# Kernel optimization log

Hardware: AMD Instinct MI355X
Metric: run time of the kernel (lower is better)

## Reference

```python
import jax, jax.numpy as jnp
import numpy as np

B, D, H, L, E, NL, P, IMG, NT = 32, 768, 8, 6, 8, 256, 16, 224, 10
G = IMG // P          # 14 patches per side
NP = G * G            # 196 patches
HD = D // H           # 96 head dim
TOPK = 2
KEEP = 0.25
EPS = 1e-5


def layer_norm(x, g, b):
    m = x.mean(-1, keepdims=True)
    v = ((x - m) ** 2).mean(-1, keepdims=True)
    return (x - m) / jnp.sqrt(v + EPS) * g + b


def mha(q, kv, in_w, in_b, out_w, out_b):
    # torch nn.MultiheadAttention: packed in_proj (3D, D), out_proj (D, D)
    wq, wk, wv = in_w[:D], in_w[D:2 * D], in_w[2 * D:]
    bq, bk, bv = in_b[:D], in_b[D:2 * D], in_b[2 * D:]

    def heads(x, w, b):
        y = x @ w.T + b                               # (B, S, D)
        return y.reshape(x.shape[0], x.shape[1], H, HD).transpose(0, 2, 1, 3)

    Q = heads(q, wq, bq)
    K = heads(kv, wk, bk)
    V = heads(kv, wv, bv)
    scores = jnp.einsum('bhqd,bhkd->bhqk', Q, K) / np.sqrt(HD).astype(np.float32)
    attn = jax.nn.softmax(scores, axis=-1)
    o = jnp.einsum('bhqk,bhkd->bhqd', attn, V)
    o = o.transpose(0, 2, 1, 3).reshape(q.shape[0], q.shape[1], D)
    return o @ out_w.T + out_b


def moe(x, rw, rb, w1, b1, w2, b2):
    # top-2 routing; renormalize the top-k weights with a second softmax
    Bq, S, _ = x.shape
    T = Bq * S
    xt = x.reshape(T, D)
    probs = jax.nn.softmax(xt @ rw.T + rb, axis=-1)       # (T, E)
    tw, ti = jax.lax.top_k(probs, TOPK)                   # (T, K)
    tw = jax.nn.softmax(tw, axis=-1)
    # combine weights per expert: (T, E), >0 only for the chosen experts
    combine = (jax.nn.one_hot(ti, E, dtype=x.dtype) * tw[..., None]).sum(axis=1)
    out = jnp.zeros_like(xt)
    for e in range(E):  # fixed small expert count
        h = jax.nn.gelu(xt @ w1[e].T + b1[e], approximate=False)
        out = out + (h @ w2[e].T + b2[e]) * combine[:, e:e + 1]
    return out.reshape(Bq, S, D)


def _forward(images, type_ids, mask_noise, conv_w, conv_b, pos_emb, type_emb,
             latents, ca_in_w, ca_in_b, ca_out_w, ca_out_b, ca_ln_g, ca_ln_b,
             sa_in_w, sa_in_b, sa_out_w, sa_out_b, ln1_g, ln1_b,
             router_w, router_b, e_w1, e_b1, e_w2, e_b2, ln2_g, ln2_b):
    b = images.shape[0]
    # non-overlapping conv patch embed == unfold + matmul
    xp = images.reshape(b, 3, G, P, G, P).transpose(0, 2, 4, 1, 3, 5)
    xp = xp.reshape(b, NP, 3 * P * P)
    patches = xp @ conv_w.reshape(D, -1).T + conv_b        # (B, NP, D)
    patches = patches + pos_emb + type_emb[type_ids][:, None, :]
    # random masking: keep n_visible patches chosen by argsort of noise
    n_visible = int(NP * KEEP)
    order = jnp.argsort(mask_noise, axis=1)
    visible_indices = order[:, :n_visible]
    masked_indices = order[:, n_visible:]
    visible = jnp.take_along_axis(patches, visible_indices[:, :, None], axis=1)
    # cross attention from latents to visible patches
    lat = jnp.broadcast_to(latents, (b, NL, D))
    lat = layer_norm(lat + mha(lat, visible, ca_in_w, ca_in_b, ca_out_w, ca_out_b),
                     ca_ln_g, ca_ln_b)
    for l in range(L):
        a = mha(lat, lat, sa_in_w[l], sa_in_b[l], sa_out_w[l], sa_out_b[l])
        lat = layer_norm(lat + a, ln1_g[l], ln1_b[l])
        m = moe(lat, router_w[l], router_b[l], e_w1[l], e_b1[l], e_w2[l], e_b2[l])
        lat = layer_norm(lat + m, ln2_g[l], ln2_b[l])
    return lat, visible_indices, masked_indices


def setup_inputs() -> dict:
    key = jax.random.key(0)
    ks = jax.random.split(key, 16)
    r = lambda k, shape, s=0.02: jax.random.normal(k, shape, dtype=jnp.float32) * s
    z = lambda shape: jnp.zeros(shape, jnp.float32)
    o = lambda shape: jnp.ones(shape, jnp.float32)
    inp = {}
    inp['images'] = jax.random.normal(ks[0], (B, 3, IMG, IMG), dtype=jnp.float32)
    inp['type_ids'] = jax.random.randint(ks[1], (B,), 0, NT)
    inp['mask_noise'] = jax.random.uniform(ks[2], (B, NP), dtype=jnp.float32)
    inp['conv_w'] = r(ks[3], (D, 3, P, P))
    inp['conv_b'] = z((D,))
    inp['pos_emb'] = r(ks[4], (1, NP, D), 1.0)
    inp['type_emb'] = r(ks[5], (NT, D), 1.0)
    inp['latents'] = r(ks[6], (NL, D), 1.0)
    inp['ca_in_w'] = r(ks[7], (3 * D, D)); inp['ca_in_b'] = z((3 * D,))
    inp['ca_out_w'] = r(ks[8], (D, D)); inp['ca_out_b'] = z((D,))
    inp['ca_ln_g'] = o((D,)); inp['ca_ln_b'] = z((D,))
    inp['sa_in_w'] = r(ks[9], (L, 3 * D, D)); inp['sa_in_b'] = z((L, 3 * D))
    inp['sa_out_w'] = r(ks[10], (L, D, D)); inp['sa_out_b'] = z((L, D))
    inp['ln1_g'] = o((L, D)); inp['ln1_b'] = z((L, D))
    inp['router_w'] = r(ks[11], (L, E, D)); inp['router_b'] = z((L, E))
    inp['e_w1'] = r(ks[12], (L, E, 2 * D, D)); inp['e_b1'] = z((L, E, 2 * D))
    inp['e_w2'] = r(ks[13], (L, E, D, 2 * D)); inp['e_b2'] = z((L, E, D))
    inp['ln2_g'] = o((L, D)); inp['ln2_b'] = z((L, D))
    return inp


def reference(images, type_ids, mask_noise, conv_w, conv_b, pos_emb, type_emb,
              latents, ca_in_w, ca_in_b, ca_out_w, ca_out_b, ca_ln_g, ca_ln_b,
              sa_in_w, sa_in_b, sa_out_w, sa_out_b, ln1_g, ln1_b,
              router_w, router_b, e_w1, e_b1, e_w2, e_b2, ln2_g, ln2_b):
    return _forward(images, type_ids, mask_noise, conv_w, conv_b, pos_emb,
                    type_emb, latents, ca_in_w, ca_in_b, ca_out_w, ca_out_b,
                    ca_ln_g, ca_ln_b, sa_in_w, sa_in_b, sa_out_w, sa_out_b,
                    ln1_g, ln1_b, router_w, router_b, e_w1, e_b1, e_w2, e_b2,
                    ln2_g, ln2_b)
```

## Files before the change

kernel.cpp:

```cpp
#include <hip/hip_runtime.h>

typedef unsigned short u16;
typedef unsigned int u32;
typedef __attribute__((ext_vector_type(8))) u16 u16x8;
typedef __attribute__((ext_vector_type(8))) __bf16 bf16x8;
typedef __attribute__((ext_vector_type(4))) float f32x4;

#define DEV static __device__ __forceinline__

DEV float b2f(u16 u){ unsigned int i = ((unsigned int)u)<<16; float f; __builtin_memcpy(&f,&i,4); return f; }
DEV u16 f2b(float f){ unsigned int x; __builtin_memcpy(&x,&f,4); x = x + 0x7fffu + ((x>>16)&1u); return (u16)(x>>16); }

DEV void gll16(const u16* g, u16* l){
    __builtin_amdgcn_global_load_lds(
        (const __attribute__((address_space(1))) u32*)(const void*)g,
        (__attribute__((address_space(3))) u32*)(void*)l, 16, 0, 0);
}

template<bool F32>
DEV u16x8 ld8(const void* base, long off){
    if constexpr (F32){
        const float* p = (const float*)base + off;
        float4 a = *(const float4*)p;
        float4 b = *(const float4*)(p+4);
        u16x8 r;
        r[0]=f2b(a.x); r[1]=f2b(a.y); r[2]=f2b(a.z); r[3]=f2b(a.w);
        r[4]=f2b(b.x); r[5]=f2b(b.y); r[6]=f2b(b.z); r[7]=f2b(b.w);
        return r;
    } else {
        return *(const u16x8*)((const u16*)base + off);
    }
}
template<bool F32>
DEV const void* vadd(const void* p, long elems){
    if constexpr (F32) return (const void*)((const float*)p + elems);
    else               return (const void*)((const u16*)p + elems);
}

#define LAT_ELEMS 6291456
#define NVIS 49
#define NMASK 147
#define T_TOK 8192
#define MOE_CAP 17408
#define MOE_HALF 8704
#define KOFF 6291456L
#define VOFF 12582912L

__global__ __launch_bounds__(256) void wconv(const float* __restrict__ src, u16* __restrict__ dst, long n)
{
    long i = ((long)blockIdx.x*256 + threadIdx.x)*8;
    if (i >= n) return;
    *(u16x8*)(dst + i) = ld8<true>(src, i);
}

__global__ __launch_bounds__(256) void argsort_k(const float* __restrict__ noise,
                                                 int* __restrict__ order,
                                                 float* __restrict__ dout)
{
    __shared__ float vals[196];
    __shared__ int ord[196];
    int b = blockIdx.x, tid = threadIdx.x;
    if (tid < 196) vals[tid] = noise[b*196 + tid];
    __syncthreads();
    if (tid < 196){
        float vi = vals[tid]; int rank = 0;
        for (int j=0;j<196;j++){ float vj = vals[j]; rank += (vj < vi) || (vj == vi && j < tid); }
        ord[rank] = tid;
    }
    __syncthreads();
    if (tid < 196){
        int v = ord[tid];
        order[b*196 + tid] = v;
        if (tid < NVIS) dout[LAT_ELEMS + b*NVIS + tid] = (float)v;
        else            dout[LAT_ELEMS + 32*NVIS + b*NMASK + (tid - NVIS)] = (float)v;
    }
}

__global__ __launch_bounds__(256) void patch_gather(const float* __restrict__ images,
                                                    const int* __restrict__ order,
                                                    u16* __restrict__ Ap)
{
    int i = blockIdx.x*256 + threadIdx.x;
    int t = i/48, kc = i - t*48;
    if (t >= 1664) return;
    if (t >= 1568){
        u16x8 z{};
        *(u16x8*)(Ap + (long)t*768 + kc*16)     = z;
        *(u16x8*)(Ap + (long)t*768 + kc*16 + 8) = z;
        return;
    }
    int b = t/49, vi = t - b*49;
    int p = order[b*196 + vi];
    int c = kc >> 4, py = kc & 15;
    int gy = p/14, gx = p - gy*14;
    const float* src = images + (((long)(b*3 + c)*224 + gy*16 + py)*224 + gx*16);
    u16x8 o0 = ld8<true>(src, 0);
    u16x8 o1 = ld8<true>(src, 8);
    *(u16x8*)(Ap + (long)t*768 + kc*16)     = o0;
    *(u16x8*)(Ap + (long)t*768 + kc*16 + 8) = o1;
}

__global__ __launch_bounds__(256) void add_pos_type(u16* __restrict__ vis,
                                                    const int* __restrict__ order,
                                                    const int* __restrict__ type_ids,
                                                    const float* __restrict__ pos,
                                                    const float* __restrict__ temb)
{
    int i = blockIdx.x*256 + threadIdx.x;
    int t = i/96, dc = (i - t*96)*8;
    if (t >= 1568) return;
    int b = t/49, vi = t - b*49;
    int p = order[b*196 + vi], tb = type_ids[b];
    u16x8 a = *(u16x8*)(vis + (long)t*768 + dc);
    const float* pp = pos  + (long)p*768 + dc;
    const float* tt = temb + (long)tb*768 + dc;
    float4 p0 = *(const float4*)pp, p1 = *(const float4*)(pp+4);
    float4 t0 = *(const float4*)tt, t1 = *(const float4*)(tt+4);
    u16x8 o;
    o[0]=f2b(b2f(a[0])+p0.x+t0.x); o[1]=f2b(b2f(a[1])+p0.y+t0.y);
    o[2]=f2b(b2f(a[2])+p0.z+t0.z); o[3]=f2b(b2f(a[3])+p0.w+t0.w);
    o[4]=f2b(b2f(a[4])+p1.x+t1.x); o[5]=f2b(b2f(a[5])+p1.y+t1.y);
    o[6]=f2b(b2f(a[6])+p1.z+t1.z); o[7]=f2b(b2f(a[7])+p1.w+t1.w);
    *(u16x8*)(vis + (long)t*768 + dc) = o;
}

template<int BK, bool BIAS, bool GELU, int GRP, bool AF32, bool BF32, bool SWZ, bool GLL>
__global__ __launch_bounds__(256,4) void gemm_nt(
    const void* __restrict__ A, const void* __restrict__ B, const float* __restrict__ bias,
    u16* __restrict__ C,
    int M, int N, int K, int lda, int ldb, int ldc,
    float scale, int ZLO, int NB,
    long sAh, long sAl, long sBh, long sBl, long sCh, long sCl,
    const int* __restrict__ aoff, const int* __restrict__ tos, const u16* __restrict__ zbuf,
    int row_base, long sBE, long sBiasE)
{
    int bx = blockIdx.x, by = blockIdx.y;
    if (SWZ){
        int nx = gridDim.x, ny = gridDim.y;
        int nwg = nx*ny;
        int flat = by*nx + bx;
        int q = nwg >> 3, r = nwg & 7;
        int xcd = flat & 7, idx = flat >> 3;
        int wg = (xcd < r ? xcd*(q+1) : r*(q+1) + (xcd - r)*q) + idx;
        bx = wg % nx; by = wg / nx;
    }
    int z = blockIdx.z; int zh = z / ZLO, zl = z - zh*ZLO;
    const void* Ab = vadd<AF32>(A, zh*sAh + zl*sAl);
    const void* Bb = vadd<BF32>(B, zh*sBh + zl*sBl);
    u16* Cb = C + zh*sCh + zl*sCl;
    const float* biasb = bias;
    int row0 = by*128, col0 = bx*128;
    int lim = 0;
    if (GRP == 1 || GRP == 2){
        lim = aoff[8];
        int g0 = row_base + row0;
        if (g0 >= lim) return;
        int e = 0;
        #pragma unroll
        for (int i=1;i<8;i++) if (g0 >= aoff[i]) e = i;
        Bb = vadd<BF32>(B, (long)e*sBE);
        if (BIAS) biasb = bias + (long)e*sBiasE;
    }
    constexpr int SP = GLL ? BK : BK + 8;
    __shared__ __align__(16) u16 As[128*SP];
    __shared__ __align__(16) u16 Bs[128*SP];
    int tid = threadIdx.x;
    int lane = tid & 63, wv = tid >> 6;
    int wr = (wv>>1)*64, wc = (wv&1)*64;
    f32x4 acc[4][4];
    #pragma unroll
    for (int m=0;m<4;m++){
        #pragma unroll
        for (int n=0;n<4;n++) acc[m][n] = f32x4{0.f,0.f,0.f,0.f};
    }
    constexpr int RPC = BK/8;
    constexpr int RPI = 64/RPC;
    constexpr int NJ  = 32/RPI;
    constexpr int PER = 128*RPC/256;
    int tA[4];
    if (GRP == 1){
        if (GLL){
            #pragma unroll
            for (int j=0;j<NJ;j++){
                int r = wv*32 + j*RPI + (lane/RPC);
                tA[j] = tos[row_base + row0 + r];
            }
        } else {
            #pragma unroll
            for (int j=0;j<PER && j<4;j++){
                int c = j*256 + tid;
                tA[j] = tos[row_base + row0 + c/RPC];
            }
        }
    }
    for (int k0=0; k0<K; k0+=BK){
        if constexpr (GLL){
            #pragma unroll
            for (int j=0;j<NJ;j++){
                int r  = wv*32 + j*RPI + (lane/RPC);
                int ch = lane % RPC;
                const u16* sa;
                if (GRP == 1){
                    int t = tA[j];
                    sa = (t >= 0) ? (const u16*)Ab + (long)t*lda + k0 + ch*8 : zbuf + ch*8;
                } else {
                    sa = (const u16*)Ab + (long)(row0+r)*lda + k0 + ch*8;
                }
                gll16(sa, As + (wv*32 + j*RPI)*BK);
                const u16* sb = (col0 + r < NB) ? (const u16*)Bb + (long)(col0+r)*ldb + k0 + ch*8
                                                : zbuf + ch*8;
                gll16(sb, Bs + (wv*32 + j*RPI)*BK);
            }
        } else {
            #pragma unroll
            for (int j=0;j<PER;j++){
                int c = j*256 + tid;
                int r = c / RPC, cc = (c - r*RPC)*8;
                u16x8 va{}, vb{};
                if (GRP == 1){
                    int t = tA[j];
                    if (t >= 0) va = ld8<AF32>(Ab, (long)t*lda + k0 + cc);
                } else {
                    va = ld8<AF32>(Ab, (long)(row0+r)*lda + k0 + cc);
                }
                if (col0 + r < NB) vb = ld8<BF32>(Bb, (long)(col0+r)*ldb + k0 + cc);
                *(u16x8*)(As + r*SP + cc) = va;
                *(u16x8*)(Bs + r*SP + cc) = vb;
            }
        }
        __syncthreads();
        #pragma unroll
        for (int kk=0; kk<BK/32; kk++){
            bf16x8 af[4], bg[4];
            #pragma unroll
            for (int m=0;m<4;m++)
                af[m] = *(const bf16x8*)(As + (wr + m*16 + (lane&15))*SP + kk*32 + (lane>>4)*8);
            #pragma unroll
            for (int n=0;n<4;n++)
                bg[n] = *(const bf16x8*)(Bs + (wc + n*16 + (lane&15))*SP + kk*32 + (lane>>4)*8);
            #pragma unroll
            for (int m=0;m<4;m++){
                #pragma unroll
                for (int n=0;n<4;n++)
                    acc[m][n] = __builtin_amdgcn_mfma_f32_16x16x32_bf16(af[m], bg[n], acc[m][n], 0,0,0);
            }
        }
        __syncthreads();
    }
    #pragma unroll
    for (int m=0;m<4;m++){
        int rbase = row0 + wr + m*16 + ((lane>>4)<<2);
        #pragma unroll
        for (int n=0;n<4;n++){
            int col = col0 + wc + n*16 + (lane&15);
            if (col < N){
                float bv = BIAS ? biasb[col] : 0.f;
                #pragma unroll
                for (int j=0;j<4;j++){
                    int row = rbase + j;
                    bool ok = (row < M);
                    if (GRP == 1 || GRP == 2) ok = ok && (row_base + row) < lim;
                    if (ok){
                        float v = acc[m][n][j]*scale + bv;
                        if (GELU) v = 0.5f*v*(1.f + erff(v*0.70710678118f));
                        u16 ov = f2b(v);
                        if (GRP == 3){
                            if (col < 768){
                                Cb[(long)row*768 + col] = ov;
                            } else if (col < 1536){
                                Cb[sBE + (long)row*768 + (col - 768)] = ov;
                            } else {
                                int c96 = col - 1536;
                                int h = c96/96, d = c96 - h*96;
                                Cb[sBiasE + ((long)((row>>8)*8 + h)*96 + d)*256 + (row & 255)] = ov;
                            }
                        } else if (GRP == 2){
                            Cb[(long)(row_base + row)*ldc + col] = ov;
                        } else {
                            Cb[(long)row*ldc + col] = ov;
                        }
                    }
                }
            }
        }
    }
}

__global__ __launch_bounds__(256) void ca_attn(const u16* __restrict__ Qc,
                                               const u16* __restrict__ KV,
                                               u16* __restrict__ attn_out)
{
    __shared__ float Sm[256*49];
    __shared__ u16 KVs[49*96];
    int b = blockIdx.x, h = blockIdx.y, q = threadIdx.x;
    for (int i=q; i<49*96; i+=256){ int k=i/96, d=i-k*96; KVs[i] = KV[(long)(b*49+k)*1536 + h*96 + d]; }
    __syncthreads();
    float qv[96];
    #pragma unroll
    for (int d=0;d<96;d++) qv[d] = b2f(Qc[(long)q*768 + h*96 + d]);
    for (int k=0;k<49;k++){
        float a = 0.f;
        #pragma unroll
        for (int d=0;d<96;d++) a += qv[d]*b2f(KVs[k*96+d]);
        Sm[q*49+k] = a*0.10206207f;
    }
    __syncthreads();
    for (int i=q; i<49*96; i+=256){ int k=i/96, d=i-k*96; KVs[i] = KV[(long)(b*49+k)*1536 + 768 + h*96 + d]; }
    float mx = -1e30f;
    for (int k=0;k<49;k++) mx = fmaxf(mx, Sm[q*49+k]);
    float sum = 0.f;
    for (int k=0;k<49;k++){ float e = __expf(Sm[q*49+k]-mx); Sm[q*49+k]=e; sum+=e; }
    float inv = 1.f/sum;
    __syncthreads();
    for (int d=0;d<96;d++){
        float a = 0.f;
        for (int k=0;k<49;k++) a += Sm[q*49+k]*b2f(KVs[k*96+d]);
        attn_out[(long)(b*256+q)*768 + h*96 + d] = f2b(a*inv);
    }
}

__global__ __launch_bounds__(256) void softmax256(u16* __restrict__ S, int rows)
{
    int wid = threadIdx.x >> 6, lane = threadIdx.x & 63;
    int r = blockIdx.x*4 + wid; if (r >= rows) return;
    u16* p = S + (long)r*256;
    ushort4 v = *(const ushort4*)(p + lane*4);
    float x0=b2f(v.x), x1=b2f(v.y), x2=b2f(v.z), x3=b2f(v.w);
    float mx = fmaxf(fmaxf(x0,x1), fmaxf(x2,x3));
    #pragma unroll
    for (int off=32; off>=1; off>>=1) mx = fmaxf(mx, __shfl_xor(mx, off, 64));
    x0=__expf(x0-mx); x1=__expf(x1-mx); x2=__expf(x2-mx); x3=__expf(x3-mx);
    float s = x0+x1+x2+x3;
    #pragma unroll
    for (int off=32; off>=1; off>>=1) s += __shfl_xor(s, off, 64);
    float inv = 1.f/s;
    ushort4 o; o.x=f2b(x0*inv); o.y=f2b(x1*inv); o.z=f2b(x2*inv); o.w=f2b(x3*inv);
    *(ushort4*)(p + lane*4) = o;
}

template<int MODE>
__global__ __launch_bounds__(256) void ln_k(
    const float* __restrict__ res, int resmod,
    const u16* __restrict__ add,
    const u16* __restrict__ OutE, const int* __restrict__ sot, const float2* __restrict__ w01,
    const float* __restrict__ g, const float* __restrict__ bb,
    float* __restrict__ out, u16* __restrict__ outb, int T)
{
    int wid = threadIdx.x >> 6, lane = threadIdx.x & 63;
    int t = blockIdx.x*4 + wid; if (t >= T) return;
    const float* rp = res + (long)(t % resmod)*768;
    float x[12];
    #pragma unroll
    for (int j=0;j<3;j++){
        float4 v = *(const float4*)(rp + j*256 + lane*4);
        x[j*4+0]=v.x; x[j*4+1]=v.y; x[j*4+2]=v.z; x[j*4+3]=v.w;
    }
    if (MODE == 0){
        const u16* ap = add + (long)t*768;
        #pragma unroll
        for (int j=0;j<3;j++){
            ushort4 v = *(const ushort4*)(ap + j*256 + lane*4);
            x[j*4+0]+=b2f(v.x); x[j*4+1]+=b2f(v.y); x[j*4+2]+=b2f(v.z); x[j*4+3]+=b2f(v.w);
        }
    } else {
        int s0 = sot[2*t], s1 = sot[2*t+1];
        float2 w = w01[t];
        const u16* p0 = OutE + (long)s0*768;
        const u16* p1 = OutE + (long)s1*768;
        #pragma unroll
        for (int j=0;j<3;j++){
            ushort4 v0 = *(const ushort4*)(p0 + j*256 + lane*4);
            ushort4 v1 = *(const ushort4*)(p1 + j*256 + lane*4);
            x[j*4+0] += w.x*b2f(v0.x) + w.y*b2f(v1.x);
            x[j*4+1] += w.x*b2f(v0.y) + w.y*b2f(v1.y);
            x[j*4+2] += w.x*b2f(v0.z) + w.y*b2f(v1.z);
            x[j*4+3] += w.x*b2f(v0.w) + w.y*b2f(v1.w);
        }
    }
    float s = 0.f;
    #pragma unroll
    for (int i=0;i<12;i++) s += x[i];
    #pragma unroll
    for (int off=32; off>=1; off>>=1) s += __shfl_xor(s, off, 64);
    float m = s*(1.f/768.f);
    float s2 = 0.f;
    #pragma unroll
    for (int i=0;i<12;i++){ float d = x[i]-m; s2 += d*d; }
    #pragma unroll
    for (int off=32; off>=1; off>>=1) s2 += __shfl_xor(s2, off, 64);
    float rstd = rsqrtf(s2*(1.f/768.f) + 1e-5f);
    #pragma unroll
    for (int j=0;j<3;j++){
        int col = j*256 + lane*4;
        float4 gg = *(const float4*)(g + col);
        float4 bv = *(const float4*)(bb + col);
        float4 o;
        o.x = (x[j*4+0]-m)*rstd*gg.x + bv.x;
        o.y = (x[j*4+1]-m)*rstd*gg.y + bv.y;
        o.z = (x[j*4+2]-m)*rstd*gg.z + bv.z;
        o.w = (x[j*4+3]-m)*rstd*gg.w + bv.w;
        *(float4*)(out + (long)t*768 + col) = o;
        if (outb != nullptr){
            ushort4 ob;
            ob.x = f2b(o.x); ob.y = f2b(o.y); ob.z = f2b(o.z); ob.w = f2b(o.w);
            *(ushort4*)(outb + (long)t*768 + col) = ob;
        }
    }
}

__global__ __launch_bounds__(256) void router_k(const float* __restrict__ lat,
                                                const float* __restrict__ rw, const float* __restrict__ rb,
                                                int2* __restrict__ e01, float2* __restrict__ w01)
{
    int wid = threadIdx.x >> 6, lane = threadIdx.x & 63;
    int t = blockIdx.x*4 + wid; if (t >= T_TOK) return;
    const float* lp = lat + (long)t*768;
    float4 x[3];
    #pragma unroll
    for (int j=0;j<3;j++) x[j] = *(const float4*)(lp + j*256 + lane*4);
    float part[8];
    #pragma unroll
    for (int e=0;e<8;e++){
        const float* wp = rw + e*768;
        float a = 0.f;
        #pragma unroll
        for (int j=0;j<3;j++){
            float4 w4 = *(const float4*)(wp + j*256 + lane*4);
            a += x[j].x*w4.x + x[j].y*w4.y + x[j].z*w4.z + x[j].w*w4.w;
        }
        part[e] = a;
    }
    #pragma unroll
    for (int e=0;e<8;e++){
        #pragma unroll
        for (int off=32; off>=1; off>>=1) part[e] += __shfl_xor(part[e], off, 64);
    }
    if (lane == 0){
        float pe[8];
        float mx = -1e30f;
        #pragma unroll
        for (int e=0;e<8;e++){ pe[e] = part[e] + rb[e]; mx = fmaxf(mx, pe[e]); }
        float sum = 0.f;
        #pragma unroll
        for (int e=0;e<8;e++){ pe[e] = __expf(pe[e]-mx); sum += pe[e]; }
        float inv = 1.f/sum;
        #pragma unroll
        for (int e=0;e<8;e++) pe[e] *= inv;
        int i0 = 0;
        #pragma unroll
        for (int e=1;e<8;e++) if (pe[e] > pe[i0]) i0 = e;
        int i1 = -1;
        for (int e=0;e<8;e++){ if (e == i0) continue; if (i1 < 0 || pe[e] > pe[i1]) i1 = e; }
        float ex = __expf(pe[i1] - pe[i0]);
        float w0 = 1.f/(1.f+ex), w1 = ex/(1.f+ex);
        e01[t] = int2{i0, i1};
        w01[t] = float2{w0, w1};
    }
}

__global__ __launch_bounds__(256) void route_build(const int2* __restrict__ e01,
                                                   int* __restrict__ aoff_g,
                                                   int* __restrict__ tos, int* __restrict__ sot,
                                                   u16* __restrict__ zbuf)
{
    __shared__ int wsum[8][4];
    __shared__ int wbase[8][4];
    __shared__ int aoff_s[9];
    int tid = threadIdx.x, lane = tid & 63, wid = tid >> 6;
    for (int s = tid; s < MOE_CAP; s += 256) tos[s] = -1;
    if (tid < 128) zbuf[tid] = 0;
    int t0 = tid * 32;
    int lc[8];
    #pragma unroll
    for (int e=0;e<8;e++) lc[e] = 0;
    for (int i=0;i<32;i++){
        int2 e = e01[t0+i];
        lc[e.x]++; lc[e.y]++;
    }
    int excl[8];
    #pragma unroll
    for (int e=0;e<8;e++){
        int sc = lc[e];
        #pragma unroll
        for (int off=1; off<64; off<<=1){
            int n = __shfl_up(sc, off, 64);
            if (lane >= off) sc += n;
        }
        excl[e] = sc - lc[e];
        if (lane == 63) wsum[e][wid] = sc;
    }
    __syncthreads();
    if (tid == 0){
        int tot = 0;
        #pragma unroll
        for (int e=0;e<8;e++){
            int s = 0;
            #pragma unroll
            for (int w=0;w<4;w++){ wbase[e][w] = s; s += wsum[e][w]; }
            aoff_s[e] = tot;
            tot += (s + 127) & ~127;
        }
        aoff_s[8] = tot;
        #pragma unroll
        for (int e=0;e<9;e++) aoff_g[e] = aoff_s[e];
    }
    __syncthreads();
    int cur[8];
    #pragma unroll
    for (int e=0;e<8;e++) cur[e] = aoff_s[e] + wbase[e][wid] + excl[e];
    for (int i=0;i<32;i++){
        int t = t0 + i;
        int2 e = e01[t];
        int s0 = cur[e.x]++;
        tos[s0] = t; sot[2*t]   = s0;
        int s1 = cur[e.y]++;
        tos[s1] = t; sot[2*t+1] = s1;
    }
}

extern "C" void kernel_launch(void* const* d_in, const int* in_sizes, int n_in,
                              void* d_out, int out_size, void* d_ws, size_t ws_size,
                              hipStream_t stream)
{
    (void)in_sizes; (void)n_in; (void)out_size;
    const float* images   = (const float*)d_in[0];
    const int*   type_ids = (const int*)d_in[1];
    const float* noise    = (const float*)d_in[2];
    const float* conv_w   = (const float*)d_in[3];
    const float* conv_b   = (const float*)d_in[4];
    const float* pos_emb  = (const float*)d_in[5];
    const float* type_emb = (const float*)d_in[6];
    const float* latents  = (const float*)d_in[7];
    const float* ca_in_w  = (const float*)d_in[8];
    const float* ca_in_b  = (const float*)d_in[9];
    const float* ca_out_w = (const float*)d_in[10];
    const float* ca_out_b = (const float*)d_in[11];
    const float* ca_ln_g  = (const float*)d_in[12];
    const float* ca_ln_b  = (const float*)d_in[13];
    const float* sa_in_w  = (const float*)d_in[14];
    const float* sa_in_b  = (const float*)d_in[15];
    const float* sa_out_w = (const float*)d_in[16];
    const float* sa_out_b = (const float*)d_in[17];
    const float* ln1_g    = (const float*)d_in[18];
    const float* ln1_b    = (const float*)d_in[19];
    const float* router_w = (const float*)d_in[20];
    const float* router_b = (const float*)d_in[21];
    const float* e_w1     = (const float*)d_in[22];
    const float* e_b1     = (const float*)d_in[23];
    const float* e_w2     = (const float*)d_in[24];
    const float* e_b2     = (const float*)d_in[25];
    const float* ln2_g    = (const float*)d_in[26];
    const float* ln2_b    = (const float*)d_in[27];
    float* dout = (float*)d_out;
    float* lat  = dout;

    char* p = (char*)d_ws;
    auto alloc = [&](size_t n)->char*{ char* r = p; p += (n + 255) & ~(size_t)255; return r; };
    int*    order  = (int*)   alloc(32*196*4);
    int2*   e01    = (int2*)  alloc((size_t)T_TOK*8);
    float2* w01    = (float2*)alloc((size_t)T_TOK*8);
    int*    aoff   = (int*)   alloc(64);
    int*    tos    = (int*)   alloc((size_t)MOE_CAP*4);
    int*    sot    = (int*)   alloc((size_t)T_TOK*2*4);
    u16*    zbuf   = (u16*)   alloc(256);
    size_t aux_used = (size_t)(p - (char*)d_ws);
    const size_t WB_BYTES = 92798976ull + 260702208ull;
    bool wb  = ws_size >= aux_used + WB_BYTES;
    bool big = wb || ws_size >= aux_used + 92798976ull;
    u16* ar = (u16*)alloc(wb ? WB_BYTES : (big ? 92798976ull : 71303168ull));
    u16* latb   = big ? ar : nullptr;
    u16* common = big ? ar + 6291456 : ar;
    u16* wbufA  = wb ? ar + 6291456 + 40108032 : nullptr;
    u16* Ap  = common;
    u16* vis = common + 1277952;
    u16* KV  = common + 2555904;
    u16* Qc  = common + 5111808;
    u16* caO = common + 5308416;
    u16* caM = common + 11599872;
    u16* Qb  = common;
    u16* Vt  = common + VOFF;
    u16* S   = common + 18874368;
    u16* aO  = common;
    u16* mha = common + KOFF;
    u16* Hbuf = common;
    u16* OutE = common + (big ? 26738688 : 13369344);
    u16* cwb      = wbufA;
    u16* cainb    = wbufA + 589824;
    u16* caoutb   = wbufA + 2359296;
    u16* winbAll  = wbufA + 2949120;
    u16* woutbAll = wbufA + 13565952;
    u16* w1bAll   = wbufA + 17104896;
    u16* w2bAll   = wbufA + 73728000;

    const float ONE = 1.0f;
    const float SCL = 0.10206207f;
    const long Z0 = 0;

    argsort_k<<<32, 256, 0, stream>>>(noise, order, dout);
    patch_gather<<<312, 256, 0, stream>>>(images, order, Ap);
    if (wb){
        wconv<<<288, 256, 0, stream>>>(conv_w, cwb, 589824);
        wconv<<<864, 256, 0, stream>>>(ca_in_w, cainb, 1769472);
        wconv<<<288, 256, 0, stream>>>(ca_out_w, caoutb, 589824);
        wconv<<<5184, 256, 0, stream>>>(sa_in_w, winbAll, 10616832);
        wconv<<<1728, 256, 0, stream>>>(sa_out_w, woutbAll, 3538944);
        wconv<<<27648, 256, 0, stream>>>(e_w1, w1bAll, 56623104);
        wconv<<<27648, 256, 0, stream>>>(e_w2, w2bAll, 56623104);
        gemm_nt<64,true,false,0,false,false,true,true><<<dim3(6,13,1),256,0,stream>>>(Ap, cwb, conv_b, vis,
            1664,768,768, 768,768,768, ONE, 1, 768, Z0,Z0,Z0,Z0,Z0,Z0, nullptr,nullptr,zbuf,0, Z0,Z0);
        add_pos_type<<<588, 256, 0, stream>>>(vis, order, type_ids, pos_emb, type_emb);
        gemm_nt<64,true,false,0,true,false,true,false><<<dim3(6,2,1),256,0,stream>>>(latents, cainb, ca_in_b, Qc,
            256,768,768, 768,768,768, ONE, 1, 768, Z0,Z0,Z0,Z0,Z0,Z0, nullptr,nullptr,zbuf,0, Z0,Z0);
        gemm_nt<64,true,false,0,false,false,true,true><<<dim3(12,13,1),256,0,stream>>>(vis, cainb + 589824, ca_in_b + 768, KV,
            1664,1536,768, 768,768,1536, ONE, 1, 1536, Z0,Z0,Z0,Z0,Z0,Z0, nullptr,nullptr,zbuf,0, Z0,Z0);
        ca_attn<<<dim3(32,8), 256, 0, stream>>>(Qc, KV, caO);
        gemm_nt<64,true,false,0,false,false,true,true><<<dim3(6,64,1),256,0,stream>>>(caO, caoutb, ca_out_b, caM,
            T_TOK,768,768, 768,768,768, ONE, 1, 768, Z0,Z0,Z0,Z0,Z0,Z0, nullptr,nullptr,zbuf,0, Z0,Z0);
    } else {
        gemm_nt<64,true,false,0,false,true,false,false><<<dim3(6,13,1),256,0,stream>>>(Ap, conv_w, conv_b, vis,
            1664,768,768, 768,768,768, ONE, 1, 768, Z0,Z0,Z0,Z0,Z0,Z0, nullptr,nullptr,zbuf,0, Z0,Z0);
        add_pos_type<<<588, 256, 0, stream>>>(vis, order, type_ids, pos_emb, type_emb);
        gemm_nt<64,true,false,0,true,true,false,false><<<dim3(6,2,1),256,0,stream>>>(latents, ca_in_w, ca_in_b, Qc,
            256,768,768, 768,768,768, ONE, 1, 768, Z0,Z0,Z0,Z0,Z0,Z0, nullptr,nullptr,zbuf,0, Z0,Z0);
        gemm_nt<64,true,false,0,false,true,false,false><<<dim3(12,13,1),256,0,stream>>>(vis, ca_in_w + 768*768, ca_in_b + 768, KV,
            1664,1536,768, 768,768,1536, ONE, 1, 1536, Z0,Z0,Z0,Z0,Z0,Z0, nullptr,nullptr,zbuf,0, Z0,Z0);
        ca_attn<<<dim3(32,8), 256, 0, stream>>>(Qc, KV, caO);
        gemm_nt<64,true,false,0,false,true,false,false><<<dim3(6,64,1),256,0,stream>>>(caO, ca_out_w, ca_out_b, caM,
            T_TOK,768,768, 768,768,768, ONE, 1, 768, Z0,Z0,Z0,Z0,Z0,Z0, nullptr,nullptr,zbuf,0, Z0,Z0);
    }
    ln_k<0><<<2048, 256, 0, stream>>>(latents, 256, caM, nullptr,nullptr,nullptr, ca_ln_g, ca_ln_b, lat, latb, T_TOK);

    for (int l=0; l<6; l++){
        const float* b_in  = sa_in_b  + l*2304;
        const float* b_out = sa_out_b + l*768;
        const float* b1 = e_b1 + l*8*1536;
        const float* b2 = e_b2 + l*8*768;
        if (wb){
            const u16* winb  = winbAll  + (long)l*1769472;
            const u16* woutb = woutbAll + (long)l*589824;
            const u16* w1b   = w1bAll   + (long)l*9437184;
            const u16* w2b   = w2bAll   + (long)l*9437184;
            gemm_nt<64,true,false,3,false,false,true,true><<<dim3(18,64,1),256,0,stream>>>(latb, winb, b_in, Qb,
                T_TOK,2304,768, 768,768,0, ONE, 1, 2304, Z0,Z0,Z0,Z0,Z0,Z0, nullptr,nullptr,zbuf,0, KOFF, VOFF);
            gemm_nt<32,false,false,0,false,false,false,true><<<dim3(2,2,256),256,0,stream>>>(Qb, Qb + KOFF, nullptr, S,
                256,256,96, 768,768,256, SCL, 8, 256, 196608,96, 196608,96, 524288,65536, nullptr,nullptr,zbuf,0, Z0,Z0);
            softmax256<<<16384, 256, 0, stream>>>(S, 65536);
            gemm_nt<64,false,false,0,false,false,false,true><<<dim3(1,2,256),256,0,stream>>>(S, Vt, nullptr, aO,
                256,96,256, 256,256,768, ONE, 8, 96, 524288,65536, 196608,24576, 196608,96, nullptr,nullptr,zbuf,0, Z0,Z0);
            gemm_nt<64,true,false,0,false,false,true,true><<<dim3(6,64,1),256,0,stream>>>(aO, woutb, b_out, mha,
                T_TOK,768,768, 768,768,768, ONE, 1, 768, Z0,Z0,Z0,Z0,Z0,Z0, nullptr,nullptr,zbuf,0, Z0,Z0);
            ln_k<0><<<2048, 256, 0, stream>>>(lat, T_TOK, mha, nullptr,nullptr,nullptr, ln1_g + l*768, ln1_b + l*768, lat, latb, T_TOK);
            router_k<<<2048, 256, 0, stream>>>(lat, router_w + l*8*768, router_b + l*8, e01, w01);
            route_build<<<1, 256, 0, stream>>>(e01, aoff, tos, sot, zbuf);
            gemm_nt<64,true,true,1,false,false,true,true><<<dim3(12,136,1),256,0,stream>>>(latb, w1b, b1, Hbuf,
                MOE_CAP,1536,768, 768,768,1536, ONE, 1, 1536, Z0,Z0,Z0,Z0,Z0,Z0,
                aoff, tos, zbuf, 0, (long)1536*768, 1536);
            gemm_nt<64,true,false,2,false,false,true,true><<<dim3(6,136,1),256,0,stream>>>(Hbuf, w2b, b2, OutE,
                MOE_CAP,768,1536, 1536,1536,768, ONE, 1, 768, Z0,Z0,Z0,Z0,Z0,Z0,
                aoff, tos, zbuf, 0, (long)768*1536, 768);
            ln_k<1><<<2048, 256, 0, stream>>>(lat, T_TOK, nullptr, OutE, sot, w01, ln2_g + l*768, ln2_b + l*768, lat, latb, T_TOK);
        } else {
            const float* w_in  = sa_in_w  + (long)l*2304*768;
            const float* w_out = sa_out_w + (long)l*768*768;
            const float* w1 = e_w1 + (long)l*8*1536*768;
            const float* w2 = e_w2 + (long)l*8*768*1536;
            if (big){
                gemm_nt<64,true,false,3,false,true,false,false><<<dim3(18,64,1),256,0,stream>>>(latb, w_in, b_in, Qb,
                    T_TOK,2304,768, 768,768,0, ONE, 1, 2304, Z0,Z0,Z0,Z0,Z0,Z0, nullptr,nullptr,zbuf,0, KOFF, VOFF);
            } else {
                gemm_nt<64,true,false,3,true,true,false,false><<<dim3(18,64,1),256,0,stream>>>(lat, w_in, b_in, Qb,
                    T_TOK,2304,768, 768,768,0, ONE, 1, 2304, Z0,Z0,Z0,Z0,Z0,Z0, nullptr,nullptr,zbuf,0, KOFF, VOFF);
            }
            gemm_nt<32,false,false,0,false,false,false,false><<<dim3(2,2,256),256,0,stream>>>(Qb, Qb + KOFF, nullptr, S,
                256,256,96, 768,768,256, SCL, 8, 256, 196608,96, 196608,96, 524288,65536, nullptr,nullptr,zbuf,0, Z0,Z0);
            softmax256<<<16384, 256, 0, stream>>>(S, 65536);
            gemm_nt<64,false,false,0,false,false,false,false><<<dim3(1,2,256),256,0,stream>>>(S, Vt, nullptr, aO,
                256,96,256, 256,256,768, ONE, 8, 96, 524288,65536, 196608,24576, 196608,96, nullptr,nullptr,zbuf,0, Z0,Z0);
            gemm_nt<64,true,false,0,false,true,false,false><<<dim3(6,64,1),256,0,stream>>>(aO, w_out, b_out, mha,
                T_TOK,768,768, 768,768,768, ONE, 1, 768, Z0,Z0,Z0,Z0,Z0,Z0, nullptr,nullptr,zbuf,0, Z0,Z0);
            ln_k<0><<<2048, 256, 0, stream>>>(lat, T_TOK, mha, nullptr,nullptr,nullptr, ln1_g + l*768, ln1_b + l*768, lat, latb, T_TOK);
            router_k<<<2048, 256, 0, stream>>>(lat, router_w + l*8*768, router_b + l*8, e01, w01);
            route_build<<<1, 256, 0, stream>>>(e01, aoff, tos, sot, zbuf);
            if (big){
                gemm_nt<64,true,true,1,false,true,false,false><<<dim3(12,136,1),256,0,stream>>>(latb, w1, b1, Hbuf,
                    MOE_CAP,1536,768, 768,768,1536, ONE, 1, 1536, Z0,Z0,Z0,Z0,Z0,Z0,
                    aoff, tos, zbuf, 0, (long)1536*768, 1536);
                gemm_nt<64,true,false,2,false,true,false,false><<<dim3(6,136,1),256,0,stream>>>(Hbuf, w2, b2, OutE,
                    MOE_CAP,768,1536, 1536,1536,768, ONE, 1, 768, Z0,Z0,Z0,Z0,Z0,Z0,
                    aoff, tos, zbuf, 0, (long)768*1536, 768);
            } else {
                for (int rb2=0; rb2<MOE_CAP; rb2+=MOE_HALF){
                    gemm_nt<64,true,true,1,true,true,false,false><<<dim3(12,68,1),256,0,stream>>>(lat, w1, b1, Hbuf,
                        MOE_HALF,1536,768, 768,768,1536, ONE, 1, 1536, Z0,Z0,Z0,Z0,Z0,Z0,
                        aoff, tos, zbuf, rb2, (long)1536*768, 1536);
                    gemm_nt<64,true,false,2,false,true,false,false><<<dim3(6,68,1),256,0,stream>>>(Hbuf, w2, b2, OutE,
                        MOE_HALF,768,1536, 1536,1536,768, ONE, 1, 768, Z0,Z0,Z0,Z0,Z0,Z0,
                        aoff, tos, zbuf, rb2, (long)768*1536, 768);
                }
            }
            ln_k<1><<<2048, 256, 0, stream>>>(lat, T_TOK, nullptr, OutE, sot, w01, ln2_g + l*768, ln2_b + l*768, lat, latb, T_TOK);
        }
    }
}
```

Baseline: 2.528 ms.

## Fuse attention scores with softmax and layernorm with router

Adds a dedicated MFMA kernel that computes the self-attention QK^T scores for a 128x256 tile per head and applies the row softmax in registers before writing. This replaces the separate scores GEMM and softmax256 launch and removes one round trip of the score matrix through memory. The router projection and top-2 selection move into the post-attention layernorm kernel, reusing the normalized values already in registers instead of rereading lat. It also raises the gemm occupancy hint to 5 and zeroes zbuf in argsort. The occupancy hint may force register spilling, and the fused kernel keeps a 128-entry accumulator per thread.

```diff
diff --git a/kernel.cpp b/kernel.cpp
--- a/kernel.cpp
+++ b/kernel.cpp
@@ -55,11 +55,13 @@
 
 __global__ __launch_bounds__(256) void argsort_k(const float* __restrict__ noise,
                                                  int* __restrict__ order,
-                                                 float* __restrict__ dout)
+                                                 float* __restrict__ dout,
+                                                 u16* __restrict__ zbuf)
 {
     __shared__ float vals[196];
     __shared__ int ord[196];
     int b = blockIdx.x, tid = threadIdx.x;
+    if (b == 0 && tid < 128) zbuf[tid] = 0;
     if (tid < 196) vals[tid] = noise[b*196 + tid];
     __syncthreads();
     if (tid < 196){
@@ -125,7 +127,7 @@
 }
 
 template<int BK, bool BIAS, bool GELU, int GRP, bool AF32, bool BF32, bool SWZ, bool GLL>
-__global__ __launch_bounds__(256,4) void gemm_nt(
+__global__ __launch_bounds__(256,5) void gemm_nt(
     const void* __restrict__ A, const void* __restrict__ B, const float* __restrict__ bias,
     u16* __restrict__ C,
     int M, int N, int K, int lda, int ldb, int ldc,
@@ -286,6 +288,72 @@
     }
 }
 
+__global__ __launch_bounds__(256,2) void scores_sm(const u16* __restrict__ Q,
+                                                   const u16* __restrict__ K,
+                                                   u16* __restrict__ S)
+{
+    __shared__ __align__(16) u16 As[128*32];
+    __shared__ __align__(16) u16 Bs[256*32];
+    int z = blockIdx.y;
+    int b = z >> 3, h = z & 7;
+    const u16* Ab = Q + (long)b*196608 + h*96 + (long)blockIdx.x*128*768;
+    const u16* Bb = K + (long)b*196608 + h*96;
+    int tid = threadIdx.x, lane = tid & 63, wv = tid >> 6;
+    f32x4 acc[2][16];
+    #pragma unroll
+    for (int m=0;m<2;m++){
+        #pragma unroll
+        for (int n=0;n<16;n++) acc[m][n] = f32x4{0.f,0.f,0.f,0.f};
+    }
+    int ch = lane & 3, rr = lane >> 2;
+    for (int k0=0;k0<96;k0+=32){
+        #pragma unroll
+        for (int j=0;j<2;j++){
+            int r = wv*32 + j*16 + rr;
+            gll16(Ab + (long)r*768 + k0 + ch*8, As + (wv*128 + j*64)*8);
+        }
+        #pragma unroll
+        for (int j=0;j<4;j++){
+            int r = wv*64 + j*16 + rr;
+            gll16(Bb + (long)r*768 + k0 + ch*8, Bs + (wv*256 + j*64)*8);
+        }
+        __syncthreads();
+        bf16x8 af[2];
+        #pragma unroll
+        for (int m=0;m<2;m++)
+            af[m] = *(const bf16x8*)(As + (wv*32 + m*16 + (lane&15))*32 + (lane>>4)*8);
+        #pragma unroll
+        for (int n=0;n<16;n++){
+            bf16x8 bg = *(const bf16x8*)(Bs + (n*16 + (lane&15))*32 + (lane>>4)*8);
+            acc[0][n] = __builtin_amdgcn_mfma_f32_16x16x32_bf16(af[0], bg, acc[0][n], 0,0,0);
+            acc[1][n] = __builtin_amdgcn_mfma_f32_16x16x32_bf16(af[1], bg, acc[1][n], 0,0,0);
+        }
+        __syncthreads();
+    }
+    const float SCL = 0.10206207f;
+    u16* Sz = S + (long)z*65536 + (long)blockIdx.x*128*256;
+    #pragma unroll
+    for (int m=0;m<2;m++){
+        #pragma unroll
+        for (int j=0;j<4;j++){
+            float mx = -1e30f;
+            #pragma unroll
+            for (int n=0;n<16;n++) mx = fmaxf(mx, acc[m][n][j]);
+            #pragma unroll
+            for (int off=8; off>=1; off>>=1) mx = fmaxf(mx, __shfl_xor(mx, off, 64));
+            float ev[16]; float sum = 0.f;
+            #pragma unroll
+            for (int n=0;n<16;n++){ ev[n] = __expf((acc[m][n][j]-mx)*SCL); sum += ev[n]; }
+            #pragma unroll
+            for (int off=8; off>=1; off>>=1) sum += __shfl_xor(sum, off, 64);
+            float inv = 1.f/sum;
+            int row = wv*32 + m*16 + ((lane>>4)<<2) + j;
+            #pragma unroll
+            for (int n=0;n<16;n++) Sz[(long)row*256 + n*16 + (lane&15)] = f2b(ev[n]*inv);
+        }
+    }
+}
+
 __global__ __launch_bounds__(256) void ca_attn(const u16* __restrict__ Qc,
                                                const u16* __restrict__ KV,
                                                u16* __restrict__ attn_out)
@@ -319,31 +387,14 @@
     }
 }
 
-__global__ __launch_bounds__(256) void softmax256(u16* __restrict__ S, int rows)
-{
-    int wid = threadIdx.x >> 6, lane = threadIdx.x & 63;
-    int r = blockIdx.x*4 + wid; if (r >= rows) return;
-    u16* p = S + (long)r*256;
-    ushort4 v = *(const ushort4*)(p + lane*4);
-    float x0=b2f(v.x), x1=b2f(v.y), x2=b2f(v.z), x3=b2f(v.w);
-    float mx = fmaxf(fmaxf(x0,x1), fmaxf(x2,x3));
-    #pragma unroll
-    for (int off=32; off>=1; off>>=1) mx = fmaxf(mx, __shfl_xor(mx, off, 64));
-    x0=__expf(x0-mx); x1=__expf(x1-mx); x2=__expf(x2-mx); x3=__expf(x3-mx);
-    float s = x0+x1+x2+x3;
-    #pragma unroll
-    for (int off=32; off>=1; off>>=1) s += __shfl_xor(s, off, 64);
-    float inv = 1.f/s;
-    ushort4 o; o.x=f2b(x0*inv); o.y=f2b(x1*inv); o.z=f2b(x2*inv); o.w=f2b(x3*inv);
-    *(ushort4*)(p + lane*4) = o;
-}
-
-template<int MODE>
+template<int MODE, bool ROUTE>
 __global__ __launch_bounds__(256) void ln_k(
     const float* __restrict__ res, int resmod,
     const u16* __restrict__ add,
     const u16* __restrict__ OutE, const int* __restrict__ sot, const float2* __restrict__ w01,
     const float* __restrict__ g, const float* __restrict__ bb,
+    const float* __restrict__ rw, const float* __restrict__ rb,
+    int2* __restrict__ e01o, float2* __restrict__ w01o,
     float* __restrict__ out, u16* __restrict__ outb, int T)
 {
     int wid = threadIdx.x >> 6, lane = threadIdx.x & 63;
@@ -389,16 +440,17 @@
     #pragma unroll
     for (int off=32; off>=1; off>>=1) s2 += __shfl_xor(s2, off, 64);
     float rstd = rsqrtf(s2*(1.f/768.f) + 1e-5f);
+    float y[12];
     #pragma unroll
     for (int j=0;j<3;j++){
         int col = j*256 + lane*4;
         float4 gg = *(const float4*)(g + col);
         float4 bv = *(const float4*)(bb + col);
-        float4 o;
-        o.x = (x[j*4+0]-m)*rstd*gg.x + bv.x;
-        o.y = (x[j*4+1]-m)*rstd*gg.y + bv.y;
-        o.z = (x[j*4+2]-m)*rstd*gg.z + bv.z;
-        o.w = (x[j*4+3]-m)*rstd*gg.w + bv.w;
+        y[j*4+0] = (x[j*4+0]-m)*rstd*gg.x + bv.x;
+        y[j*4+1] = (x[j*4+1]-m)*rstd*gg.y + bv.y;
+        y[j*4+2] = (x[j*4+2]-m)*rstd*gg.z + bv.z;
+        y[j*4+3] = (x[j*4+3]-m)*rstd*gg.w + bv.w;
+        float4 o; o.x=y[j*4+0]; o.y=y[j*4+1]; o.z=y[j*4+2]; o.w=y[j*4+3];
         *(float4*)(out + (long)t*768 + col) = o;
         if (outb != nullptr){
             ushort4 ob;
@@ -406,55 +458,45 @@
             *(ushort4*)(outb + (long)t*768 + col) = ob;
         }
     }
-}
-
-__global__ __launch_bounds__(256) void router_k(const float* __restrict__ lat,
-                                                const float* __restrict__ rw, const float* __restrict__ rb,
-                                                int2* __restrict__ e01, float2* __restrict__ w01)
-{
-    int wid = threadIdx.x >> 6, lane = threadIdx.x & 63;
-    int t = blockIdx.x*4 + wid; if (t >= T_TOK) return;
-    const float* lp = lat + (long)t*768;
-    float4 x[3];
-    #pragma unroll
-    for (int j=0;j<3;j++) x[j] = *(const float4*)(lp + j*256 + lane*4);
-    float part[8];
-    #pragma unroll
-    for (int e=0;e<8;e++){
-        const float* wp = rw + e*768;
-        float a = 0.f;
-        #pragma unroll
-        for (int j=0;j<3;j++){
-            float4 w4 = *(const float4*)(wp + j*256 + lane*4);
-            a += x[j].x*w4.x + x[j].y*w4.y + x[j].z*w4.z + x[j].w*w4.w;
-        }
-        part[e] = a;
-    }
-    #pragma unroll
-    for (int e=0;e<8;e++){
-        #pragma unroll
-        for (int off=32; off>=1; off>>=1) part[e] += __shfl_xor(part[e], off, 64);
-    }
-    if (lane == 0){
-        float pe[8];
-        float mx = -1e30f;
-        #pragma unroll
-        for (int e=0;e<8;e++){ pe[e] = part[e] + rb[e]; mx = fmaxf(mx, pe[e]); }
-        float sum = 0.f;
-        #pragma unroll
-        for (int e=0;e<8;e++){ pe[e] = __expf(pe[e]-mx); sum += pe[e]; }
-        float inv = 1.f/sum;
-        #pragma unroll
-        for (int e=0;e<8;e++) pe[e] *= inv;
-        int i0 = 0;
-        #pragma unroll
-        for (int e=1;e<8;e++) if (pe[e] > pe[i0]) i0 = e;
-        int i1 = -1;
-        for (int e=0;e<8;e++){ if (e == i0) continue; if (i1 < 0 || pe[e] > pe[i1]) i1 = e; }
-        float ex = __expf(pe[i1] - pe[i0]);
-        float w0 = 1.f/(1.f+ex), w1 = ex/(1.f+ex);
-        e01[t] = int2{i0, i1};
-        w01[t] = float2{w0, w1};
+    if (ROUTE){
+        float part[8];
+        #pragma unroll
+        for (int e=0;e<8;e++){
+            const float* wp = rw + e*768;
+            float a = 0.f;
+            #pragma unroll
+            for (int j=0;j<3;j++){
+                float4 w4 = *(const float4*)(wp + j*256 + lane*4);
+                a += y[j*4+0]*w4.x + y[j*4+1]*w4.y + y[j*4+2]*w4.z + y[j*4+3]*w4.w;
+            }
+            part[e] = a;
+        }
+        #pragma unroll
+        for (int e=0;e<8;e++){
+            #pragma unroll
+            for (int off=32; off>=1; off>>=1) part[e] += __shfl_xor(part[e], off, 64);
+        }
+        if (lane == 0){
+            float pe[8];
+            float mx = -1e30f;
+            #pragma unroll
+            for (int e=0;e<8;e++){ pe[e] = part[e] + rb[e]; mx = fmaxf(mx, pe[e]); }
+            float sum = 0.f;
+            #pragma unroll
+            for (int e=0;e<8;e++){ pe[e] = __expf(pe[e]-mx); sum += pe[e]; }
+            float inv = 1.f/sum;
+            #pragma unroll
+            for (int e=0;e<8;e++) pe[e] *= inv;
+            int i0 = 0;
+            #pragma unroll
+            for (int e=1;e<8;e++) if (pe[e] > pe[i0]) i0 = e;
+            int i1 = -1;
+            for (int e=0;e<8;e++){ if (e == i0) continue; if (i1 < 0 || pe[e] > pe[i1]) i1 = e; }
+            float ex = __expf(pe[i1] - pe[i0]);
+            float w0 = 1.f/(1.f+ex), w1 = ex/(1.f+ex);
+            e01o[t] = int2{i0, i1};
+            w01o[t] = float2{w0, w1};
+        }
     }
 }
 
@@ -593,10 +635,9 @@
     u16* w2bAll   = wbufA + 73728000;
 
     const float ONE = 1.0f;
-    const float SCL = 0.10206207f;
     const long Z0 = 0;
 
-    argsort_k<<<32, 256, 0, stream>>>(noise, order, dout);
+    argsort_k<<<32, 256, 0, stream>>>(noise, order, dout, zbuf);
     patch_gather<<<312, 256, 0, stream>>>(images, order, Ap);
     if (wb){
         wconv<<<288, 256, 0, stream>>>(conv_w, cwb, 589824);
@@ -628,13 +669,16 @@
         gemm_nt<64,true,false,0,false,true,false,false><<<dim3(6,64,1),256,0,stream>>>(caO, ca_out_w, ca_out_b, caM,
             T_TOK,768,768, 768,768,768, ONE, 1, 768, Z0,Z0,Z0,Z0,Z0,Z0, nullptr,nullptr,zbuf,0, Z0,Z0);
     }
-    ln_k<0><<<2048, 256, 0, stream>>>(latents, 256, caM, nullptr,nullptr,nullptr, ca_ln_g, ca_ln_b, lat, latb, T_TOK);
+    ln_k<0,false><<<2048, 256, 0, stream>>>(latents, 256, caM, nullptr,nullptr,nullptr, ca_ln_g, ca_ln_b,
+        nullptr,nullptr,nullptr,nullptr, lat, latb, T_TOK);
 
     for (int l=0; l<6; l++){
         const float* b_in  = sa_in_b  + l*2304;
         const float* b_out = sa_out_b + l*768;
         const float* b1 = e_b1 + l*8*1536;
         const float* b2 = e_b2 + l*8*768;
+        const float* rwl = router_w + l*8*768;
+        const float* rbl = router_b + l*8;
         if (wb){
             const u16* winb  = winbAll  + (long)l*1769472;
             const u16* woutb = woutbAll + (long)l*589824;
@@ -642,15 +686,13 @@
             const u16* w2b   = w2bAll   + (long)l*9437184;
             gemm_nt<64,true,false,3,false,false,true,true><<<dim3(18,64,1),256,0,stream>>>(latb, winb, b_in, Qb,
                 T_TOK,2304,768, 768,768,0, ONE, 1, 2304, Z0,Z0,Z0,Z0,Z0,Z0, nullptr,nullptr,zbuf,0, KOFF, VOFF);
-            gemm_nt<32,false,false,0,false,false,false,true><<<dim3(2,2,256),256,0,stream>>>(Qb, Qb + KOFF, nullptr, S,
-                256,256,96, 768,768,256, SCL, 8, 256, 196608,96, 196608,96, 524288,65536, nullptr,nullptr,zbuf,0, Z0,Z0);
-            softmax256<<<16384, 256, 0, stream>>>(S, 65536);
+            scores_sm<<<dim3(2,256), 256, 0, stream>>>(Qb, Qb + KOFF, S);
             gemm_nt<64,false,false,0,false,false,false,true><<<dim3(1,2,256),256,0,stream>>>(S, Vt, nullptr, aO,
                 256,96,256, 256,256,768, ONE, 8, 96, 524288,65536, 196608,24576, 196608,96, nullptr,nullptr,zbuf,0, Z0,Z0);
             gemm_nt<64,true,false,0,false,false,true,true><<<dim3(6,64,1),256,0,stream>>>(aO, woutb, b_out, mha,
                 T_TOK,768,768, 768,768,768, ONE, 1, 768, Z0,Z0,Z0,Z0,Z0,Z0, nullptr,nullptr,zbuf,0, Z0,Z0);
-            ln_k<0><<<2048, 256, 0, stream>>>(lat, T_TOK, mha, nullptr,nullptr,nullptr, ln1_g + l*768, ln1_b + l*768, lat, latb, T_TOK);
-            router_k<<<2048, 256, 0, stream>>>(lat, router_w + l*8*768, router_b + l*8, e01, w01);
+            ln_k<0,true><<<2048, 256, 0, stream>>>(lat, T_TOK, mha, nullptr,nullptr,nullptr, ln1_g + l*768, ln1_b + l*768,
+                rwl, rbl, e01, w01, lat, latb, T_TOK);
             route_build<<<1, 256, 0, stream>>>(e01, aoff, tos, sot, zbuf);
             gemm_nt<64,true,true,1,false,false,true,true><<<dim3(12,136,1),256,0,stream>>>(latb, w1b, b1, Hbuf,
                 MOE_CAP,1536,768, 768,768,1536, ONE, 1, 1536, Z0,Z0,Z0,Z0,Z0,Z0,
@@ -658,7 +700,8 @@
             gemm_nt<64,true,false,2,false,false,true,true><<<dim3(6,136,1),256,0,stream>>>(Hbuf, w2b, b2, OutE,
                 MOE_CAP,768,1536, 1536,1536,768, ONE, 1, 768, Z0,Z0,Z0,Z0,Z0,Z0,
                 aoff, tos, zbuf, 0, (long)768*1536, 768);
-            ln_k<1><<<2048, 256, 0, stream>>>(lat, T_TOK, nullptr, OutE, sot, w01, ln2_g + l*768, ln2_b + l*768, lat, latb, T_TOK);
+            ln_k<1,false><<<2048, 256, 0, stream>>>(lat, T_TOK, nullptr, OutE, sot, w01, ln2_g + l*768, ln2_b + l*768,
+                nullptr,nullptr,nullptr,nullptr, lat, latb, T_TOK);
         } else {
             const float* w_in  = sa_in_w  + (long)l*2304*768;
             const float* w_out = sa_out_w + (long)l*768*768;
@@ -671,15 +714,13 @@
                 gemm_nt<64,true,false,3,true,true,false,false><<<dim3(18,64,1),256,0,stream>>>(lat, w_in, b_in, Qb,
                     T_TOK,2304,768, 768,768,0, ONE, 1, 2304, Z0,Z0,Z0,Z0,Z0,Z0, nullptr,nullptr,zbuf,0, KOFF, VOFF);
             }
-            gemm_nt<32,false,false,0,false,false,false,false><<<dim3(2,2,256),256,0,stream>>>(Qb, Qb + KOFF, nullptr, S,
-                256,256,96, 768,768,256, SCL, 8, 256, 196608,96, 196608,96, 524288,65536, nullptr,nullptr,zbuf,0, Z0,Z0);
-            softmax256<<<16384, 256, 0, stream>>>(S, 65536);
-            gemm_nt<64,false,false,0,false,false,false,false><<<dim3(1,2,256),256,0,stream>>>(S, Vt, nullptr, aO,
+            scores_sm<<<dim3(2,256), 256, 0, stream>>>(Qb, Qb + KOFF, S);
+            gemm_nt<64,false,false,0,false,false,false,true><<<dim3(1,2,256),256,0,stream>>>(S, Vt, nullptr, aO,
                 256,96,256, 256,256,768, ONE, 8, 96, 524288,65536, 196608,24576, 196608,96, nullptr,nullptr,zbuf,0, Z0,Z0);
             gemm_nt<64,true,false,0,false,true,false,false><<<dim3(6,64,1),256,0,stream>>>(aO, w_out, b_out, mha,
                 T_TOK,768,768, 768,768,768, ONE, 1, 768, Z0,Z0,Z0,Z0,Z0,Z0, nullptr,nullptr,zbuf,0, Z0,Z0);
-            ln_k<0><<<2048, 256, 0, stream>>>(lat, T_TOK, mha, nullptr,nullptr,nullptr, ln1_g + l*768, ln1_b + l*768, lat, latb, T_TOK);
-            router_k<<<2048, 256, 0, stream>>>(lat, router_w + l*8*768, router_b + l*8, e01, w01);
+            ln_k<0,true><<<2048, 256, 0, stream>>>(lat, T_TOK, mha, nullptr,nullptr,nullptr, ln1_g + l*768, ln1_b + l*768,
+                rwl, rbl, e01, w01, lat, latb, T_TOK);
             route_build<<<1, 256, 0, stream>>>(e01, aoff, tos, sot, zbuf);
             if (big){
                 gemm_nt<64,true,true,1,false,true,false,false><<<dim3(12,136,1),256,0,stream>>>(latb, w1, b1, Hbuf,
@@ -698,7 +739,8 @@
                         aoff, tos, zbuf, rb2, (long)768*1536, 768);
                 }
             }
-            ln_k<1><<<2048, 256, 0, stream>>>(lat, T_TOK, nullptr, OutE, sot, w01, ln2_g + l*768, ln2_b + l*768, lat, latb, T_TOK);
-        }
-    }
-}
+            ln_k<1,false><<<2048, 256, 0, stream>>>(lat, T_TOK, nullptr, OutE, sot, w01, ln2_g + l*768, ln2_b + l*768,
+                nullptr,nullptr,nullptr,nullptr, lat, latb, T_TOK);
+        }
+    }
+}
```

After: 3.815 ms. +50.9%, slower.
